# Performance work log

Hardware: AMD Instinct MI355X
Metric: run time of the kernel (lower is better)

## Reference

```python
import jax, jax.numpy as jnp
import numpy as np

B, S, QS, KS, F, H = 4, 2048, 512, 1024, 1024, 16
DH = F // H  # head dim = 64


def setup_inputs() -> dict:
    key = jax.random.key(0)
    ks = jax.random.split(key, 7)
    s = 0.02
    return {
        "x": jax.random.normal(ks[0], (B, S, QS), dtype=jnp.float32),
        "y": jax.random.normal(ks[1], (B, S, QS), dtype=jnp.float32),
        "z": jax.random.normal(ks[2], (B, S, KS), dtype=jnp.float32),
        "Wq": jax.random.normal(ks[3], (2 * QS, F), dtype=jnp.float32) * s,
        "Wk": jax.random.normal(ks[4], (KS, F), dtype=jnp.float32) * s,
        "Wv": jax.random.normal(ks[5], (KS, F), dtype=jnp.float32) * s,
        "Wo": jax.random.normal(ks[6], (F, F), dtype=jnp.float32) * s,
    }


def _split_heads(t):
    # [B, S, F] -> [B, H, S, DH]
    return t.reshape(B, S, H, DH).transpose(0, 2, 1, 3)


def reference(x, y, z, Wq, Wk, Wv, Wo):
    q = _split_heads(jnp.concatenate([x, y], axis=-1) @ Wq)  # [B,H,S,DH]
    k = _split_heads(z @ Wk)
    v = _split_heads(z @ Wv)
    scale = 1.0 / jnp.sqrt(jnp.asarray(DH, dtype=q.dtype))
    scores = jnp.einsum("bhsd,bhtd->bhst", q, k) * scale  # [B,H,S,S]
    attn = jax.nn.softmax(scores, axis=-1)
    out = jnp.einsum("bhst,bhtd->bhsd", attn, v)  # [B,H,S,DH]
    out = out.transpose(0, 2, 1, 3).reshape(B, S, F)
    return out @ Wo
```

## Files before the change

### kernel.cpp

```cpp
#include <hip/hip_runtime.h>

typedef __attribute__((ext_vector_type(8))) short short8;
typedef __attribute__((ext_vector_type(4))) float f32x4;
typedef __attribute__((ext_vector_type(16))) float f32x16;
typedef __attribute__((ext_vector_type(4))) unsigned short us4;
typedef __attribute__((ext_vector_type(4))) unsigned int u32x4;

#define GLOAD16(gsrc, ldst)                                             \
  __builtin_amdgcn_global_load_lds(                                     \
      (const __attribute__((address_space(1))) unsigned int*)(gsrc),    \
      (__attribute__((address_space(3))) unsigned int*)(ldst), 16, 0, 0)

#define VMEM_DRAIN_BARRIER()                              \
  do {                                                    \
    asm volatile("s_waitcnt vmcnt(0)" ::: "memory");      \
    __builtin_amdgcn_sched_barrier(0);                    \
    __syncthreads();                                      \
  } while (0)

#if __has_builtin(__builtin_amdgcn_exp2f)
#define EXP2F(x) __builtin_amdgcn_exp2f(x)
#else
#define EXP2F(x) exp2f(x)
#endif

static __device__ __forceinline__ unsigned short f2bf(float f) {
  unsigned int u = __float_as_uint(f);
  u += 0x7fffu + ((u >> 16) & 1u);
  return (unsigned short)(u >> 16);
}

static __device__ __forceinline__ unsigned cvtpk(float lo, float hi) {
  unsigned r;
  asm("v_cvt_pk_bf16_f32 %0, %1, %2" : "=v"(r) : "v"(lo), "v"(hi));
  return r;
}

__global__ __launch_bounds__(256) void conv_in(const float* __restrict__ x,
                                               const float* __restrict__ y,
                                               const float* __restrict__ z,
                                               unsigned short* __restrict__ XY,
                                               unsigned short* __restrict__ Z) {
  const int NX = (8192 * 512) / 4;
  const int NZ = (8192 * 1024) / 4;
  const int total = 2 * NX + NZ;
  for (int idx = blockIdx.x * blockDim.x + threadIdx.x; idx < total;
       idx += gridDim.x * blockDim.x) {
    const float* src;
    unsigned short* dst;
    if (idx < NX) {
      int p = idx * 4; int row = p >> 9, c = p & 511;
      src = x + p; dst = XY + (size_t)row * 1024 + c;
    } else if (idx < 2 * NX) {
      int p = (idx - NX) * 4; int row = p >> 9, c = p & 511;
      src = y + p; dst = XY + (size_t)row * 1024 + 512 + c;
    } else {
      int p = (idx - 2 * NX) * 4;
      src = z + p; dst = Z + p;
    }
    float4 v = *(const float4*)src;
    us4 o; o[0] = f2bf(v.x); o[1] = f2bf(v.y); o[2] = f2bf(v.z); o[3] = f2bf(v.w);
    *(us4*)dst = o;
  }
}

__global__ __launch_bounds__(256) void wT_kernel(const float* __restrict__ W,
                                                 unsigned short* __restrict__ WT) {
  __shared__ __align__(16) unsigned short LT[64 * 72];
  const int k0 = blockIdx.y * 64, n0 = blockIdx.x * 64;
  const int t = threadIdx.x;
#pragma unroll
  for (int j = 0; j < 4; ++j) {
    int r = j * 16 + (t >> 4);
    int c = (t & 15) * 4;
    float4 w = *(const float4*)(W + (size_t)(k0 + r) * 1024 + n0 + c);
    LT[(c + 0) * 72 + r] = f2bf(w.x);
    LT[(c + 1) * 72 + r] = f2bf(w.y);
    LT[(c + 2) * 72 + r] = f2bf(w.z);
    LT[(c + 3) * 72 + r] = f2bf(w.w);
  }
  __syncthreads();
#pragma unroll
  for (int j = 0; j < 2; ++j) {
    int n = j * 32 + (t >> 3), ch = t & 7;
    *(short8*)(WT + (size_t)(n0 + n) * 1024 + k0 + ch * 8) =
        *(const short8*)(LT + n * 72 + ch * 8);
  }
}

__global__ __launch_bounds__(256) void qkv_gemm(const unsigned short* __restrict__ XY,
                                                const unsigned short* __restrict__ Zb,
                                                const unsigned short* __restrict__ WqT,
                                                const unsigned short* __restrict__ WkT,
                                                const unsigned short* __restrict__ WvT,
                                                unsigned short* __restrict__ Qb,
                                                unsigned short* __restrict__ Kb,
                                                unsigned short* __restrict__ Vb) {
  __shared__ __align__(16) unsigned short As[128 * 32];
  __shared__ __align__(16) unsigned short Bs[128 * 32];
  const int tid = threadIdx.x;
  const int lane = tid & 63, wid = tid >> 6;
  const int lq = lane & 15, lg = lane >> 4;
  const int wr = wid >> 1, wc = wid & 1;
  const int seg = blockIdx.x >> 3;
  const int m0 = blockIdx.y * 128, n0 = (blockIdx.x & 7) * 128;

  const unsigned short* A;
  const unsigned short* Bt;
  unsigned short* C;
  float scale;
  if (seg == 0)      { A = XY; Bt = WqT; C = Qb; scale = 0.18033688011112042f; }
  else if (seg == 1) { A = Zb; Bt = WkT; C = Kb; scale = 1.0f; }
  else               { A = Zb; Bt = WvT; C = Vb; scale = 1.0f; }

  const int sr = tid >> 2, sc = tid & 3;
  f32x4 acc[4][4] = {};

  for (int k0 = 0; k0 < 1024; k0 += 32) {
    __syncthreads();
#pragma unroll
    for (int i = 0; i < 2; ++i) {
      int r = i * 64 + sr;
      int c = sc ^ ((r >> 1) & 3);
      GLOAD16(A + (size_t)(m0 + r) * 1024 + k0 + c * 8, (char*)As + wid * 1024 + i * 4096);
      GLOAD16(Bt + (size_t)(n0 + r) * 1024 + k0 + c * 8, (char*)Bs + wid * 1024 + i * 4096);
    }
    VMEM_DRAIN_BARRIER();
    short8 af[4], bfr[4];
#pragma unroll
    for (int mf = 0; mf < 4; ++mf) {
      int r = wr * 64 + mf * 16 + lq;
      int c = lg ^ ((r >> 1) & 3);
      af[mf] = *(const short8*)(As + r * 32 + c * 8);
    }
#pragma unroll
    for (int nf = 0; nf < 4; ++nf) {
      int r = wc * 64 + nf * 16 + lq;
      int c = lg ^ ((r >> 1) & 3);
      bfr[nf] = *(const short8*)(Bs + r * 32 + c * 8);
    }
#pragma unroll
    for (int mf = 0; mf < 4; ++mf)
#pragma unroll
      for (int nf = 0; nf < 4; ++nf)
        acc[mf][nf] = __builtin_amdgcn_mfma_f32_16x16x32_bf16(af[mf], bfr[nf],
                                                              acc[mf][nf], 0, 0, 0);
  }

#pragma unroll
  for (int mf = 0; mf < 4; ++mf)
#pragma unroll
    for (int nf = 0; nf < 4; ++nf)
#pragma unroll
      for (int j = 0; j < 4; ++j) {
        int row = m0 + wr * 64 + mf * 16 + lg * 4 + j;
        int col = n0 + wc * 64 + nf * 16 + lq;
        C[(size_t)row * 1024 + col] = f2bf(acc[mf][nf][j] * scale);
      }
}

__global__ __launch_bounds__(256) void gemm_nt(const unsigned short* __restrict__ A,
                                               const unsigned short* __restrict__ Bt,
                                               float* __restrict__ Cout) {
  __shared__ __align__(16) unsigned short As[128 * 32];
  __shared__ __align__(16) unsigned short Bs[128 * 32];
  const int tid = threadIdx.x;
  const int lane = tid & 63, wid = tid >> 6;
  const int lq = lane & 15, lg = lane >> 4;
  const int wr = wid >> 1, wc = wid & 1;
  const int m0 = blockIdx.y * 128, n0 = blockIdx.x * 128;
  const int sr = tid >> 2, sc = tid & 3;

  f32x4 acc[4][4] = {};

  for (int k0 = 0; k0 < 1024; k0 += 32) {
    __syncthreads();
#pragma unroll
    for (int i = 0; i < 2; ++i) {
      int r = i * 64 + sr;
      int c = sc ^ ((r >> 1) & 3);
      GLOAD16(A + (size_t)(m0 + r) * 1024 + k0 + c * 8, (char*)As + wid * 1024 + i * 4096);
      GLOAD16(Bt + (size_t)(n0 + r) * 1024 + k0 + c * 8, (char*)Bs + wid * 1024 + i * 4096);
    }
    VMEM_DRAIN_BARRIER();
    short8 af[4], bfr[4];
#pragma unroll
    for (int mf = 0; mf < 4; ++mf) {
      int r = wr * 64 + mf * 16 + lq;
      int c = lg ^ ((r >> 1) & 3);
      af[mf] = *(const short8*)(As + r * 32 + c * 8);
    }
#pragma unroll
    for (int nf = 0; nf < 4; ++nf) {
      int r = wc * 64 + nf * 16 + lq;
      int c = lg ^ ((r >> 1) & 3);
      bfr[nf] = *(const short8*)(Bs + r * 32 + c * 8);
    }
#pragma unroll
    for (int mf = 0; mf < 4; ++mf)
#pragma unroll
      for (int nf = 0; nf < 4; ++nf)
        acc[mf][nf] = __builtin_amdgcn_mfma_f32_16x16x32_bf16(af[mf], bfr[nf],
                                                              acc[mf][nf], 0, 0, 0);
  }

#pragma unroll
  for (int mf = 0; mf < 4; ++mf)
#pragma unroll
    for (int nf = 0; nf < 4; ++nf)
#pragma unroll
      for (int j = 0; j < 4; ++j) {
        int row = m0 + wr * 64 + mf * 16 + lg * 4 + j;
        int col = n0 + wc * 64 + nf * 16 + lq;
        Cout[(size_t)row * 1024 + col] = acc[mf][nf][j];
      }
}

__global__ __launch_bounds__(256) void vtrans(const unsigned short* __restrict__ V,
                                              unsigned short* __restrict__ Vt) {
  __shared__ __align__(16) unsigned short LT[64 * 72];
  const int bh = blockIdx.y, b = bh >> 4, h = bh & 15;
  const int s0 = blockIdx.x * 64;
  const int t = threadIdx.x;
#pragma unroll
  for (int i = 0; i < 2; ++i) {
    int r = i * 32 + (t >> 3);
    int c = t & 7;
    short8 v = *(const short8*)(V + (size_t)(b * 2048 + s0 + r) * 1024 + h * 64 + c * 8);
#pragma unroll
    for (int e = 0; e < 8; ++e)
      LT[(c * 8 + e) * 72 + r] = (unsigned short)v[e];
  }
  __syncthreads();
#pragma unroll
  for (int i = 0; i < 2; ++i) {
    int d = i * 32 + (t >> 3);
    int c = t & 7;
    *(short8*)(Vt + ((size_t)bh * 64 + d) * 2048 + s0 + c * 8) =
        *(const short8*)(LT + d * 72 + c * 8);
  }
}

__global__ __launch_bounds__(256, 4) void attn5(const unsigned short* __restrict__ Q,
                                                const unsigned short* __restrict__ K,
                                                const unsigned short* __restrict__ Vt,
                                                unsigned short* __restrict__ AO) {
  __shared__ __align__(16) unsigned short Ks[2][64 * 64];
  __shared__ __align__(16) unsigned short Vs[2][64 * 64];

  const int bh = blockIdx.y, b = bh >> 4, h = bh & 15;
  const int q0 = blockIdx.x * 128;
  const int tid = threadIdx.x, lane = tid & 63, w = tid >> 6;
  const int l31 = lane & 31, hi = lane >> 5;
  const int swz = l31 & 7;

  short8 qf[4];
#pragma unroll
  for (int dblk = 0; dblk < 4; ++dblk)
    qf[dblk] = *(const short8*)(Q + (size_t)(b * 2048 + q0 + w * 32 + l31) * 1024 +
                                h * 64 + dblk * 16 + hi * 8);

#define STAGE(bf, t)                                                               \
  do {                                                                             \
    _Pragma("unroll")                                                              \
    for (int i = 0; i < 2; ++i) {                                                  \
      int ch = i * 256 + tid;                                                      \
      int r = ch >> 3, c = ch & 7, g = c ^ (r & 7);                                \
      GLOAD16(K + (size_t)(b * 2048 + (t) * 64 + r) * 1024 + h * 64 + g * 8,       \
              (char*)Ks[bf] + i * 4096 + w * 1024);                                \
    }                                                                              \
    _Pragma("unroll")                                                              \
    for (int i = 0; i < 2; ++i) {                                                  \
      int ch = i * 256 + tid;                                                      \
      int r = ch >> 3, c = ch & 7, g = c ^ (r & 7);                                \
      GLOAD16(Vt + ((size_t)bh * 64 + r) * 2048 + (t) * 64 + g * 8,                \
              (char*)Vs[bf] + i * 4096 + w * 1024);                                \
    }                                                                              \
  } while (0)

  STAGE(0, 0);
  VMEM_DRAIN_BARRIER();

  f32x16 od[2] = {};
  float lrow = 0.f;
  int buf = 0;

  for (int t = 0; t < 32; ++t) {
    if (t < 31) STAGE(buf ^ 1, t + 1);

    f32x16 st[2];
    __builtin_amdgcn_s_setprio(1);
#pragma unroll
    for (int kh = 0; kh < 2; ++kh) {
      f32x16 a = {};
#pragma unroll
      for (int dblk = 0; dblk < 4; ++dblk) {
        short8 kf = *(const short8*)(Ks[buf] + (kh * 32 + l31) * 64 +
                                     (((dblk * 2 + hi) ^ swz) * 8));
        a = __builtin_amdgcn_mfma_f32_32x32x16_bf16(kf, qf[dblk], a, 0, 0, 0);
      }
      st[kh] = a;
    }
    __builtin_amdgcn_s_setprio(0);

    float lacc[4] = {0.f, 0.f, 0.f, 0.f};
#pragma unroll
    for (int kh = 0; kh < 2; ++kh)
#pragma unroll
      for (int r = 0; r < 16; ++r) {
        float p = EXP2F(st[kh][r]);
        st[kh][r] = p;
        lacc[r & 3] += p;
      }
    lrow += (lacc[0] + lacc[1]) + (lacc[2] + lacc[3]);

    __builtin_amdgcn_s_setprio(1);
#pragma unroll
    for (int ks = 0; ks < 4; ++ks) {
      const int tt = ks >> 1, cm = (ks & 1) * 2;
      unsigned a_lo = cvtpk(st[tt][cm * 4 + 0], st[tt][cm * 4 + 1]);
      unsigned a_hi = cvtpk(st[tt][cm * 4 + 2], st[tt][cm * 4 + 3]);
      unsigned b_lo = cvtpk(st[tt][cm * 4 + 4], st[tt][cm * 4 + 5]);
      unsigned b_hi = cvtpk(st[tt][cm * 4 + 6], st[tt][cm * 4 + 7]);
      unsigned snd_lo = hi ? a_lo : b_lo;
      unsigned snd_hi = hi ? a_hi : b_hi;
      unsigned rcv_lo = (unsigned)__shfl_xor((int)snd_lo, 32);
      unsigned rcv_hi = (unsigned)__shfl_xor((int)snd_hi, 32);
      u32x4 up;
      up[0] = hi ? rcv_lo : a_lo;
      up[1] = hi ? rcv_hi : a_hi;
      up[2] = hi ? b_lo : rcv_lo;
      up[3] = hi ? b_hi : rcv_hi;
      short8 pa = __builtin_bit_cast(short8, up);
#pragma unroll
      for (int td = 0; td < 2; ++td) {
        short8 vf = *(const short8*)(Vs[buf] + (td * 32 + l31) * 64 +
                                     (((ks * 2 + hi) ^ swz) * 8));
        od[td] = __builtin_amdgcn_mfma_f32_32x32x16_bf16(vf, pa, od[td], 0, 0, 0);
      }
    }
    __builtin_amdgcn_s_setprio(0);

    VMEM_DRAIN_BARRIER();
    buf ^= 1;
  }

  float inv = 1.0f / (lrow + __shfl_xor(lrow, 32));
  const size_t orow = (size_t)(b * 2048 + q0 + w * 32 + l31);
#pragma unroll
  for (int td = 0; td < 2; ++td)
#pragma unroll
    for (int rh = 0; rh < 4; ++rh) {
      us4 o4;
#pragma unroll
      for (int rl = 0; rl < 4; ++rl) o4[rl] = f2bf(od[td][rh * 4 + rl] * inv);
      *(us4*)(AO + orow * 1024 + h * 64 + td * 32 + rh * 8 + hi * 4) = o4;
    }
#undef STAGE
}

extern "C" void kernel_launch(void* const* d_in, const int* in_sizes, int n_in,
                              void* d_out, int out_size, void* d_ws, size_t ws_size,
                              hipStream_t stream) {
  const float* x = (const float*)d_in[0];
  const float* y = (const float*)d_in[1];
  const float* z = (const float*)d_in[2];
  const float* Wq = (const float*)d_in[3];
  const float* Wk = (const float*)d_in[4];
  const float* Wv = (const float*)d_in[5];
  const float* Wo = (const float*)d_in[6];

  char* ws = (char*)d_ws;
  unsigned short* XY  = (unsigned short*)(ws + 0);
  unsigned short* Zb  = (unsigned short*)(ws + 16777216);
  unsigned short* WqT = (unsigned short*)(ws + 33554432);
  unsigned short* WkT = (unsigned short*)(ws + 35651584);
  unsigned short* WvT = (unsigned short*)(ws + 37748736);
  unsigned short* WoT = (unsigned short*)(ws + 39845888);
  unsigned short* Qb  = (unsigned short*)(ws + 41943040);
  unsigned short* Kb  = (unsigned short*)(ws + 58720256);
  unsigned short* Vb  = (unsigned short*)(ws + 75497472);
  unsigned short* Vtg = (unsigned short*)(ws + 92274688);
  unsigned short* AO  = (unsigned short*)(ws + 109051904);

  conv_in<<<2048, 256, 0, stream>>>(x, y, z, XY, Zb);
  wT_kernel<<<dim3(16, 16), 256, 0, stream>>>(Wq, WqT);
  wT_kernel<<<dim3(16, 16), 256, 0, stream>>>(Wk, WkT);
  wT_kernel<<<dim3(16, 16), 256, 0, stream>>>(Wv, WvT);
  wT_kernel<<<dim3(16, 16), 256, 0, stream>>>(Wo, WoT);

  qkv_gemm<<<dim3(24, 64), 256, 0, stream>>>(XY, Zb, WqT, WkT, WvT, Qb, Kb, Vb);

  vtrans<<<dim3(32, 64), 256, 0, stream>>>(Vb, Vtg);
  attn5<<<dim3(16, 64), 256, 0, stream>>>(Qb, Kb, Vtg, AO);

  gemm_nt<<<dim3(8, 64), 256, 0, stream>>>(AO, WoT, (float*)d_out);
}
```

Before: 224.7 us.

## Merge prep kernels, compute softmax row sums via MFMA, use permlane32 swap

Merges the input conversion and the four weight-transpose launches into one prep kernel, so there are fewer launches and tail gaps. In attention, the row sums of the exponentiated scores are now taken from an extra MFMA against a ones vector instead of VALU adds. The cross-half exchange of the P fragments uses permlane32_swap instead of shuffles and selects. This shifts work from VALU to the matrix unit, at the cost of one extra MFMA per k-step and some extra accumulator registers.

```diff
diff --git a/kernel.cpp b/kernel.cpp
--- a/kernel.cpp
+++ b/kernel.cpp
@@ -36,39 +36,51 @@
   return r;
 }
 
-__global__ __launch_bounds__(256) void conv_in(const float* __restrict__ x,
-                                               const float* __restrict__ y,
-                                               const float* __restrict__ z,
-                                               unsigned short* __restrict__ XY,
-                                               unsigned short* __restrict__ Z) {
-  const int NX = (8192 * 512) / 4;
-  const int NZ = (8192 * 1024) / 4;
-  const int total = 2 * NX + NZ;
-  for (int idx = blockIdx.x * blockDim.x + threadIdx.x; idx < total;
-       idx += gridDim.x * blockDim.x) {
-    const float* src;
-    unsigned short* dst;
-    if (idx < NX) {
-      int p = idx * 4; int row = p >> 9, c = p & 511;
-      src = x + p; dst = XY + (size_t)row * 1024 + c;
-    } else if (idx < 2 * NX) {
-      int p = (idx - NX) * 4; int row = p >> 9, c = p & 511;
-      src = y + p; dst = XY + (size_t)row * 1024 + 512 + c;
-    } else {
-      int p = (idx - 2 * NX) * 4;
-      src = z + p; dst = Z + p;
-    }
-    float4 v = *(const float4*)src;
-    us4 o; o[0] = f2bf(v.x); o[1] = f2bf(v.y); o[2] = f2bf(v.z); o[3] = f2bf(v.w);
-    *(us4*)dst = o;
-  }
-}
-
-__global__ __launch_bounds__(256) void wT_kernel(const float* __restrict__ W,
-                                                 unsigned short* __restrict__ WT) {
+__global__ __launch_bounds__(256) void prep(const float* __restrict__ x,
+                                            const float* __restrict__ y,
+                                            const float* __restrict__ z,
+                                            const float* __restrict__ Wq,
+                                            const float* __restrict__ Wk,
+                                            const float* __restrict__ Wv,
+                                            const float* __restrict__ Wo,
+                                            unsigned short* __restrict__ XY,
+                                            unsigned short* __restrict__ Z,
+                                            unsigned short* __restrict__ WqT,
+                                            unsigned short* __restrict__ WkT,
+                                            unsigned short* __restrict__ WvT,
+                                            unsigned short* __restrict__ WoT) {
   __shared__ __align__(16) unsigned short LT[64 * 72];
-  const int k0 = blockIdx.y * 64, n0 = blockIdx.x * 64;
-  const int t = threadIdx.x;
+  const int bid = blockIdx.x, t = threadIdx.x;
+
+  if (bid < 2048) {
+    const int NX = (8192 * 512) / 4;
+    const int NZ = (8192 * 1024) / 4;
+    const int total = 2 * NX + NZ;
+    for (int idx = bid * 256 + t; idx < total; idx += 2048 * 256) {
+      const float* src;
+      unsigned short* dst;
+      if (idx < NX) {
+        int p = idx * 4; int row = p >> 9, c = p & 511;
+        src = x + p; dst = XY + (size_t)row * 1024 + c;
+      } else if (idx < 2 * NX) {
+        int p = (idx - NX) * 4; int row = p >> 9, c = p & 511;
+        src = y + p; dst = XY + (size_t)row * 1024 + 512 + c;
+      } else {
+        int p = (idx - 2 * NX) * 4;
+        src = z + p; dst = Z + p;
+      }
+      float4 v = *(const float4*)src;
+      us4 o; o[0] = f2bf(v.x); o[1] = f2bf(v.y); o[2] = f2bf(v.z); o[3] = f2bf(v.w);
+      *(us4*)dst = o;
+    }
+    return;
+  }
+
+  const int seg = (bid - 2048) >> 8;
+  const int local = (bid - 2048) & 255;
+  const float* W = (seg == 0) ? Wq : (seg == 1) ? Wk : (seg == 2) ? Wv : Wo;
+  unsigned short* WT = (seg == 0) ? WqT : (seg == 1) ? WkT : (seg == 2) ? WvT : WoT;
+  const int k0 = (local >> 4) * 64, n0 = (local & 15) * 64;
 #pragma unroll
   for (int j = 0; j < 4; ++j) {
     int r = j * 16 + (t >> 4);
@@ -241,7 +253,7 @@
   }
 }
 
-__global__ __launch_bounds__(256, 4) void attn5(const unsigned short* __restrict__ Q,
+__global__ __launch_bounds__(256, 4) void attn6(const unsigned short* __restrict__ Q,
                                                 const unsigned short* __restrict__ K,
                                                 const unsigned short* __restrict__ Vt,
                                                 unsigned short* __restrict__ AO) {
@@ -259,6 +271,10 @@
   for (int dblk = 0; dblk < 4; ++dblk)
     qf[dblk] = *(const short8*)(Q + (size_t)(b * 2048 + q0 + w * 32 + l31) * 1024 +
                                 h * 64 + dblk * 16 + hi * 8);
+
+  short8 ones;
+#pragma unroll
+  for (int e = 0; e < 8; ++e) ones[e] = (short)0x3F80;
 
 #define STAGE(bf, t)                                                               \
   do {                                                                             \
@@ -282,7 +298,7 @@
   VMEM_DRAIN_BARRIER();
 
   f32x16 od[2] = {};
-  float lrow = 0.f;
+  f32x16 sums = {};
   int buf = 0;
 
   for (int t = 0; t < 32; ++t) {
@@ -303,16 +319,10 @@
     }
     __builtin_amdgcn_s_setprio(0);
 
-    float lacc[4] = {0.f, 0.f, 0.f, 0.f};
 #pragma unroll
     for (int kh = 0; kh < 2; ++kh)
 #pragma unroll
-      for (int r = 0; r < 16; ++r) {
-        float p = EXP2F(st[kh][r]);
-        st[kh][r] = p;
-        lacc[r & 3] += p;
-      }
-    lrow += (lacc[0] + lacc[1]) + (lacc[2] + lacc[3]);
+      for (int r = 0; r < 16; ++r) st[kh][r] = EXP2F(st[kh][r]);
 
     __builtin_amdgcn_s_setprio(1);
 #pragma unroll
@@ -322,16 +332,15 @@
       unsigned a_hi = cvtpk(st[tt][cm * 4 + 2], st[tt][cm * 4 + 3]);
       unsigned b_lo = cvtpk(st[tt][cm * 4 + 4], st[tt][cm * 4 + 5]);
       unsigned b_hi = cvtpk(st[tt][cm * 4 + 6], st[tt][cm * 4 + 7]);
-      unsigned snd_lo = hi ? a_lo : b_lo;
-      unsigned snd_hi = hi ? a_hi : b_hi;
-      unsigned rcv_lo = (unsigned)__shfl_xor((int)snd_lo, 32);
-      unsigned rcv_hi = (unsigned)__shfl_xor((int)snd_hi, 32);
+      auto Xlo = __builtin_amdgcn_permlane32_swap(a_lo, b_lo, false, false);
+      auto Xhi = __builtin_amdgcn_permlane32_swap(a_hi, b_hi, false, false);
       u32x4 up;
-      up[0] = hi ? rcv_lo : a_lo;
-      up[1] = hi ? rcv_hi : a_hi;
-      up[2] = hi ? b_lo : rcv_lo;
-      up[3] = hi ? b_hi : rcv_hi;
+      up[0] = Xlo[0];
+      up[1] = Xhi[0];
+      up[2] = Xlo[1];
+      up[3] = Xhi[1];
       short8 pa = __builtin_bit_cast(short8, up);
+      sums = __builtin_amdgcn_mfma_f32_32x32x16_bf16(ones, pa, sums, 0, 0, 0);
 #pragma unroll
       for (int td = 0; td < 2; ++td) {
         short8 vf = *(const short8*)(Vs[buf] + (td * 32 + l31) * 64 +
@@ -345,7 +354,7 @@
     buf ^= 1;
   }
 
-  float inv = 1.0f / (lrow + __shfl_xor(lrow, 32));
+  float inv = 1.0f / sums[0];
   const size_t orow = (size_t)(b * 2048 + q0 + w * 32 + l31);
 #pragma unroll
   for (int td = 0; td < 2; ++td)
@@ -383,16 +392,13 @@
   unsigned short* Vtg = (unsigned short*)(ws + 92274688);
   unsigned short* AO  = (unsigned short*)(ws + 109051904);
 
-  conv_in<<<2048, 256, 0, stream>>>(x, y, z, XY, Zb);
-  wT_kernel<<<dim3(16, 16), 256, 0, stream>>>(Wq, WqT);
-  wT_kernel<<<dim3(16, 16), 256, 0, stream>>>(Wk, WkT);
-  wT_kernel<<<dim3(16, 16), 256, 0, stream>>>(Wv, WvT);
-  wT_kernel<<<dim3(16, 16), 256, 0, stream>>>(Wo, WoT);
+  prep<<<3072, 256, 0, stream>>>(x, y, z, Wq, Wk, Wv, Wo,
+                                 XY, Zb, WqT, WkT, WvT, WoT);
 
   qkv_gemm<<<dim3(24, 64), 256, 0, stream>>>(XY, Zb, WqT, WkT, WvT, Qb, Kb, Vb);
 
   vtrans<<<dim3(32, 64), 256, 0, stream>>>(Vb, Vtg);
-  attn5<<<dim3(16, 64), 256, 0, stream>>>(Qb, Kb, Vtg, AO);
+  attn6<<<dim3(16, 64), 256, 0, stream>>>(Qb, Kb, Vtg, AO);
 
   gemm_nt<<<dim3(8, 64), 256, 0, stream>>>(AO, WoT, (float*)d_out);
 }
```

Measured after the change: 217.8 us. 1.03x faster.
